# Optimization experiments

Measured on AMD Instinct MI355X. Metric: run time of the kernel, lower is better.

## Reference

```python
import jax, jax.numpy as jnp
import numpy as np

DIM, NH, NKV = 1024, 16, 4
HD = DIM // NH  # 64
B, T = 2, 2048


def _rotary_freqs(seq_len, dim):
    inv_freq = 1.0 / (10000.0 ** (jnp.arange(0, dim, 2, dtype=jnp.float32) / dim))
    pos = jnp.arange(seq_len, dtype=jnp.float32)
    return pos[:, None] * inv_freq[None, :]  # [T, dim/2]


def _apply_rotary(x, freqs):
    # x: [B, H, T, HD]; freqs: [T, HD/2]
    x1, x2 = x[..., ::2], x[..., 1::2]
    cos, sin = jnp.cos(freqs), jnp.sin(freqs)
    # NOTE: faithful to source, second half is x1*sin - x2*cos (not +)
    return jnp.concatenate([x1 * cos - x2 * sin, x1 * sin - x2 * cos], axis=-1)


def setup_inputs() -> dict:
    key = jax.random.key(0)
    ks = jax.random.split(key, 5)
    s = 0.02
    return {
        "x": jax.random.normal(ks[0], (B, T, DIM), dtype=jnp.float32),
        "Wq": jax.random.normal(ks[1], (DIM, DIM), dtype=jnp.float32) * s,
        "bq": jnp.zeros((DIM,), jnp.float32),
        "Wk": jax.random.normal(ks[2], (DIM, NKV * HD), dtype=jnp.float32) * s,
        "bk": jnp.zeros((NKV * HD,), jnp.float32),
        "Wv": jax.random.normal(ks[3], (DIM, NKV * HD), dtype=jnp.float32) * s,
        "bv": jnp.zeros((NKV * HD,), jnp.float32),
        "Wo": jax.random.normal(ks[4], (DIM, DIM), dtype=jnp.float32) * s,
        "bo": jnp.zeros((DIM,), jnp.float32),
    }


def reference(x, Wq, bq, Wk, bk, Wv, bv, Wo, bo):
    Bx, Tx, C = x.shape
    q = (x @ Wq + bq).reshape(Bx, Tx, NH, HD).transpose(0, 2, 1, 3)   # [B,NH,T,HD]
    k = (x @ Wk + bk).reshape(Bx, Tx, NKV, HD).transpose(0, 2, 1, 3)  # [B,NKV,T,HD]
    v = (x @ Wv + bv).reshape(Bx, Tx, NKV, HD).transpose(0, 2, 1, 3)

    freqs = _rotary_freqs(Tx, HD)
    q = _apply_rotary(q, freqs)
    k = _apply_rotary(k, freqs)

    rep = NH // NKV
    k = jnp.repeat(k, rep, axis=1)  # [B,NH,T,HD]
    v = jnpp = jnp.repeat(v, rep, axis=1)

    scores = jnp.einsum('bhqd,bhkd->bhqk', q, k) / jnp.sqrt(jnp.float32(HD))
    causal = jnp.tril(jnp.ones((Tx, Tx), dtype=bool))
    scores = jnp.where(causal[None, None], scores, -jnp.inf)
    attn = jax.nn.softmax(scores, axis=-1)
    ctx = jnp.einsum('bhqk,bhkd->bhqd', attn, v)
    out = ctx.transpose(0, 2, 1, 3).reshape(Bx, Tx, C)
    return out @ Wo + bo
```

## Files before the change

### kernel.cpp

```cpp
#include <hip/hip_runtime.h>
#include <math.h>

#define DIM 1024
#define NH 16
#define NKV 4
#define HD 64
#define HALF 32
#define NB 2
#define SEQ 2048
#define KVD 256
#define MTOT 4096
#define QSCALE 0.18033688f
#define MBIAS 8.0f

typedef __bf16 bf16x8 __attribute__((ext_vector_type(8)));
typedef float f32x4 __attribute__((ext_vector_type(4)));
typedef unsigned short u16x8 __attribute__((ext_vector_type(8)));

#define MFMA16(a, b, c) __builtin_amdgcn_mfma_f32_16x16x32_bf16(a, b, c, 0, 0, 0)

__device__ __forceinline__ unsigned short f2bf(float f) {
    unsigned int u = __float_as_uint(f);
    u = (u + 0x7fffu + ((u >> 16) & 1u)) >> 16;
    return (unsigned short)u;
}

__device__ __forceinline__ unsigned cvt_pk(float lo, float hi) {
    unsigned r;
    asm("v_cvt_pk_bf16_f32 %0, %1, %2" : "=v"(r) : "v"(lo), "v"(hi));
    return r;
}

__device__ __forceinline__ void gll16(const unsigned short* g, unsigned short* l) {
    __builtin_amdgcn_global_load_lds((const __attribute__((address_space(1))) void*)g,
                                     (__attribute__((address_space(3))) void*)l, 16, 0, 0);
}

__global__ __launch_bounds__(256) void prep_kernel(
    const float* __restrict__ x,
    const float* __restrict__ Wq, const float* __restrict__ Wk,
    const float* __restrict__ Wv, const float* __restrict__ Wo,
    unsigned short* __restrict__ xb,
    unsigned short* __restrict__ qt, unsigned short* __restrict__ kt,
    unsigned short* __restrict__ vt, unsigned short* __restrict__ ot,
    float* __restrict__ cosb, float* __restrict__ sinb)
{
    __shared__ float tile[64][65];
    const int bx = blockIdx.x;
    const int tid = threadIdx.x;
    if (bx < 256) {
        int idx = bx * 256 + tid;
        int t = idx >> 5, d = idx & 31;
        float e = (float)(2 * d) / (float)HD;
        float invf = 1.0f / powf(10000.0f, e);
        float f = (float)t * invf;
        cosb[idx] = cosf(f);
        sinb[idx] = sinf(f);
    } else if (bx < 2304) {
        int i = ((bx - 256) * 256 + tid) * 8;
        float4 v0 = *(const float4*)&x[i];
        float4 v1 = *(const float4*)&x[i + 4];
        u16x8 o;
        o[0] = f2bf(v0.x); o[1] = f2bf(v0.y); o[2] = f2bf(v0.z); o[3] = f2bf(v0.w);
        o[4] = f2bf(v1.x); o[5] = f2bf(v1.y); o[6] = f2bf(v1.z); o[7] = f2bf(v1.w);
        *(u16x8*)&xb[i] = o;
    } else {
        int idx2 = bx - 2304;
        int z = idx2 >> 8, rem = idx2 & 255, xx = rem & 15, yy = rem >> 4;
        const float* W; unsigned short* Wt; int N;
        switch (z) {
            case 0: W = Wq; Wt = qt; N = DIM; break;
            case 1: W = Wk; Wt = kt; N = KVD; break;
            case 2: W = Wv; Wt = vt; N = KVD; break;
            default: W = Wo; Wt = ot; N = DIM; break;
        }
        const int n0 = xx * 64;
        if (n0 >= N) return;
        const int k0 = yy * 64;
        const int row = tid >> 2, coff = (tid & 3) * 16;
#pragma unroll
        for (int i = 0; i < 4; i++) {
            float4 v = *(const float4*)&W[(size_t)(k0 + row) * N + n0 + coff + i * 4];
            tile[row][coff + i * 4 + 0] = v.x; tile[row][coff + i * 4 + 1] = v.y;
            tile[row][coff + i * 4 + 2] = v.z; tile[row][coff + i * 4 + 3] = v.w;
        }
        __syncthreads();
        u16x8 a, b;
#pragma unroll
        for (int i = 0; i < 8; i++) a[i] = f2bf(tile[coff + i][row]);
#pragma unroll
        for (int i = 0; i < 8; i++) b[i] = f2bf(tile[coff + 8 + i][row]);
        *(u16x8*)&Wt[(size_t)(n0 + row) * DIM + k0 + coff] = a;
        *(u16x8*)&Wt[(size_t)(n0 + row) * DIM + k0 + coff + 8] = b;
    }
}

__global__ __launch_bounds__(256) void qkv_gemm_kernel(
    const unsigned short* __restrict__ xb,
    const unsigned short* __restrict__ wqt, const unsigned short* __restrict__ wkt,
    const unsigned short* __restrict__ wvt,
    const float* __restrict__ bq, const float* __restrict__ bk, const float* __restrict__ bv,
    const float* __restrict__ cosb, const float* __restrict__ sinb,
    unsigned short* __restrict__ qbuf, unsigned short* __restrict__ kbuf,
    unsigned short* __restrict__ vT)
{
    __shared__ unsigned short As[64 * 64];
    __shared__ unsigned short Bs[128 * 64];
    const int tid = threadIdx.x;
    const int lane = tid & 63, w = tid >> 6;
    const int l15 = lane & 15, lg = lane >> 4;
    const int bid = blockIdx.x;
    const int lid = (bid & 7) * 96 + (bid >> 3);
    const int m0 = (lid / 12) * 64;
    const int n0g = (lid % 12) * 128;

    const unsigned short* Wt; const float* bias; int n0, mode;
    if (n0g < DIM)            { Wt = wqt; bias = bq; n0 = n0g; mode = 0; }
    else if (n0g < DIM + KVD) { Wt = wkt; bias = bk; n0 = n0g - DIM; mode = 1; }
    else                      { Wt = wvt; bias = bv; n0 = n0g - DIM - KVD; mode = 2; }

    const int wr = w >> 1, wc = w & 1;

    f32x4 acc[2][4];
#pragma unroll
    for (int i = 0; i < 2; i++)
#pragma unroll
        for (int j = 0; j < 4; j++) acc[i][j] = (f32x4){0.f, 0.f, 0.f, 0.f};

    for (int k0 = 0; k0 < DIM; k0 += 64) {
        __syncthreads();
#pragma unroll
        for (int i = 0; i < 2; i++) {
            int S = i * 256 + tid;
            int r = S >> 3, qd = S & 7;
            gll16(xb + (size_t)(m0 + r) * DIM + k0 + ((qd ^ (r & 7)) * 8),
                  &As[(i * 256 + (tid & ~63)) * 8]);
        }
#pragma unroll
        for (int i = 0; i < 4; i++) {
            int S = i * 256 + tid;
            int r = S >> 3, qd = S & 7;
            gll16(Wt + (size_t)(n0 + r) * DIM + k0 + ((qd ^ (r & 7)) * 8),
                  &Bs[(i * 256 + (tid & ~63)) * 8]);
        }
        __syncthreads();
        bf16x8 af[2][2], bfr[4][2];
#pragma unroll
        for (int r = 0; r < 2; r++) {
            const int row = wr * 32 + r * 16 + l15;
#pragma unroll
            for (int kk = 0; kk < 2; kk++)
                af[r][kk] = *(const bf16x8*)&As[row * 64 + (((kk * 4 + lg) ^ (row & 7)) << 3)];
        }
#pragma unroll
        for (int c = 0; c < 4; c++) {
            const int row = wc * 64 + c * 16 + l15;
#pragma unroll
            for (int kk = 0; kk < 2; kk++)
                bfr[c][kk] = *(const bf16x8*)&Bs[row * 64 + (((kk * 4 + lg) ^ (row & 7)) << 3)];
        }
#pragma unroll
        for (int kk = 0; kk < 2; kk++)
#pragma unroll
            for (int r = 0; r < 2; r++)
#pragma unroll
                for (int c = 0; c < 4; c++)
                    acc[r][c] = MFMA16(af[r][kk], bfr[c][kk], acc[r][c]);
    }

    const int nloc = n0 + wc * 64;
    const bool even = (l15 & 1) == 0;
#pragma unroll
    for (int rt = 0; rt < 2; rt++) {
#pragma unroll
        for (int ct = 0; ct < 4; ct++) {
            const int c = ct * 16 + l15;
            const float bsv = bias[nloc + c];
            if (mode == 2) {
                const int col = nloc + c;
                const int khh = col >> 6, d = col & 63;
                const int bb = m0 >> 11;
                const int t = (m0 & (SEQ - 1)) + wr * 32 + rt * 16 + lg * 4;
                float v0 = acc[rt][ct][0] + bsv;
                float v1 = acc[rt][ct][1] + bsv;
                float v2 = acc[rt][ct][2] + bsv;
                float v3 = acc[rt][ct][3] + bsv;
                unsigned short* dst = vT + ((size_t)(bb * NKV + khh) * 64 + d) * SEQ + t;
                *(uint2*)dst = make_uint2(cvt_pk(v0, v1), cvt_pk(v2, v3));
            } else {
                const int p = c >> 1;
#pragma unroll
                for (int q = 0; q < 4; q++) {
                    const int mrow = m0 + wr * 32 + rt * 16 + lg * 4 + q;
                    float val = acc[rt][ct][q] + bsv;
                    float prt = __shfl_xor(val, 1);
                    const int t = mrow & (SEQ - 1);
                    float cs = cosb[t * HALF + p];
                    float sn = sinb[t * HALF + p];
                    float outv = even ? (val * cs - prt * sn) : (prt * sn - val * cs);
                    int outc = even ? p : (p + 32);
                    if (mode == 0) qbuf[(size_t)mrow * DIM + nloc + outc] = f2bf(outv * QSCALE);
                    else           kbuf[(size_t)mrow * KVD + nloc + outc] = f2bf(outv);
                }
            }
        }
    }
}

__global__ __launch_bounds__(256, 4) void attn_mfma_kernel(
    const unsigned short* __restrict__ qb, const unsigned short* __restrict__ kb,
    const unsigned short* __restrict__ vT, unsigned short* __restrict__ ctx)
{
    __shared__ unsigned short Ks[2][64 * 64];
    __shared__ unsigned short Vt[2][64 * 64];
    __shared__ unsigned Pw[4][16 * 32];

    const int tid = threadIdx.x;
    const int lane = tid & 63, w = tid >> 6;
    const int l15 = lane & 15, lg = lane >> 4;
    const int h = blockIdx.y;
    const int b = blockIdx.z;
    const int kh = h >> 2;
    const int g = h + NH * b;
    const int v = (blockIdx.x + g) & 31;
    const int r_ = v & 7, k_ = v >> 3;
    const int tile = (k_ == 0) ? r_ : (k_ == 1) ? (r_ + 8) : (k_ == 2) ? (31 - r_) : (23 - r_);
    const int q0 = tile * 64;

    const unsigned short* kg = kb + (size_t)b * SEQ * KVD + (size_t)kh * HD;
    const unsigned short* vg = vT + ((size_t)(b * NKV + kh) * HD) * SEQ;

    const int qg_row = w * 16 + l15;
    const int swzd = (l15 & 7) << 3;
    unsigned* PW = &Pw[w][l15 * 32];
    const int pswz = (l15 & 7) << 2;

    const unsigned short* qptr = qb + ((size_t)(b * SEQ + q0 + qg_row) * DIM + h * HD + lg * 8);
    bf16x8 bq0 = *(const bf16x8*)qptr;
    bf16x8 bq1 = *(const bf16x8*)(qptr + 32);

    const int S1 = w * 64 + lane, r1 = S1 >> 3, d81 = ((S1 & 7) ^ (r1 & 7)) * 8;
    const int S2 = 256 + w * 64 + lane, r2 = S2 >> 3, d82 = ((S2 & 7) ^ (r2 & 7)) * 8;

    gll16(kg + (size_t)r1 * KVD + d81, &Ks[0][(w * 64) * 8]);
    gll16(vg + (size_t)r1 * SEQ + d81, &Vt[0][(w * 64) * 8]);
    gll16(kg + (size_t)r2 * KVD + d82, &Ks[0][(256 + w * 64) * 8]);
    gll16(vg + (size_t)r2 * SEQ + d82, &Vt[0][(256 + w * 64) * 8]);
    __syncthreads();

    f32x4 o[4];
#pragma unroll
    for (int i = 0; i < 4; i++) o[i] = (f32x4){0.f, 0.f, 0.f, 0.f};
    float lrun = 0.f;

    const int nch = tile + 1;
#pragma unroll 1
    for (int ch = 0; ch < nch; ch++) {
        const int cur = ch & 1;
        if (ch + 1 < nch) {
            const int kv1 = (ch + 1) * 64;
            gll16(kg + (size_t)(kv1 + r1) * KVD + d81, &Ks[cur ^ 1][(w * 64) * 8]);
            gll16(vg + (size_t)r1 * SEQ + kv1 + d81,   &Vt[cur ^ 1][(w * 64) * 8]);
            gll16(kg + (size_t)(kv1 + r2) * KVD + d82, &Ks[cur ^ 1][(256 + w * 64) * 8]);
            gll16(vg + (size_t)r2 * SEQ + kv1 + d82,   &Vt[cur ^ 1][(256 + w * 64) * 8]);
        }

        f32x4 sacc[4];
#pragma unroll
        for (int i = 0; i < 4; i++) sacc[i] = (f32x4){0.f, 0.f, 0.f, 0.f};
        __builtin_amdgcn_s_setprio(1);
#pragma unroll
        for (int ct = 0; ct < 4; ct++) {
            const int kr = ct * 16 + l15;
            bf16x8 ak = *(const bf16x8*)&Ks[cur][kr * 64 + ((lg * 8) ^ swzd)];
            sacc[ct] = MFMA16(ak, bq0, sacc[ct]);
        }
#pragma unroll
        for (int ct = 0; ct < 4; ct++) {
            const int kr = ct * 16 + l15;
            bf16x8 ak = *(const bf16x8*)&Ks[cur][kr * 64 + ((32 + lg * 8) ^ swzd)];
            sacc[ct] = MFMA16(ak, bq1, sacc[ct]);
        }
        __builtin_amdgcn_s_setprio(0);

        if (ch == nch - 1) {
#pragma unroll
            for (int ct = 0; ct < 4; ct++)
#pragma unroll
                for (int r = 0; r < 4; r++)
                    if (ct * 16 + lg * 4 + r > qg_row) sacc[ct][r] = -INFINITY;
        }

        float rs = 0.f;
        unsigned pk0[4], pk1[4];
#pragma unroll
        for (int ct = 0; ct < 4; ct++) {
            float p0 = exp2f(sacc[ct][0] - MBIAS);
            float p1 = exp2f(sacc[ct][1] - MBIAS);
            float p2 = exp2f(sacc[ct][2] - MBIAS);
            float p3 = exp2f(sacc[ct][3] - MBIAS);
            rs += (p0 + p1) + (p2 + p3);
            pk0[ct] = cvt_pk(p0, p1);
            pk1[ct] = cvt_pk(p2, p3);
        }
        lrun += rs;

#pragma unroll
        for (int ct = 0; ct < 4; ct++) {
            int wrd = (ct * 8 + lg * 2) ^ pswz;
            *(uint2*)&PW[wrd] = make_uint2(pk0[ct], pk1[ct]);
        }

        __builtin_amdgcn_s_setprio(1);
#pragma unroll
        for (int s = 0; s < 2; s++) {
            int wrd = (s * 16 + lg * 4) ^ pswz;
            bf16x8 ap = *(const bf16x8*)&PW[wrd];
#pragma unroll
            for (int dt = 0; dt < 4; dt++) {
                const int d = dt * 16 + l15;
                bf16x8 bv2 = *(const bf16x8*)&Vt[cur][d * 64 + ((s * 32 + lg * 8) ^ ((d & 7) << 3))];
                o[dt] = MFMA16(ap, bv2, o[dt]);
            }
        }
        __builtin_amdgcn_s_setprio(0);

        __syncthreads();
    }

    lrun += __shfl_xor(lrun, 16);
    lrun += __shfl_xor(lrun, 32);
    float linv = 1.0f / lrun;
    float lb0 = __shfl(linv, lg * 4 + 0);
    float lb1 = __shfl(linv, lg * 4 + 1);
    float lb2 = __shfl(linv, lg * 4 + 2);
    float lb3 = __shfl(linv, lg * 4 + 3);
#pragma unroll
    for (int dt = 0; dt < 4; dt++) {
        const size_t base = (size_t)(b * SEQ + q0 + w * 16 + lg * 4) * DIM + h * HD + dt * 16 + l15;
        ctx[base]           = f2bf(o[dt][0] * lb0);
        ctx[base + DIM]     = f2bf(o[dt][1] * lb1);
        ctx[base + 2 * DIM] = f2bf(o[dt][2] * lb2);
        ctx[base + 3 * DIM] = f2bf(o[dt][3] * lb3);
    }
}

__global__ __launch_bounds__(256) void outproj_kernel(
    const unsigned short* __restrict__ ctx, const unsigned short* __restrict__ wot,
    const float* __restrict__ bo, float* __restrict__ out)
{
    __shared__ unsigned short As[64 * 64];
    __shared__ unsigned short Bs[128 * 64];
    const int tid = threadIdx.x;
    const int lane = tid & 63, w = tid >> 6;
    const int l15 = lane & 15, lg = lane >> 4;
    const int bid = blockIdx.x;
    const int lid = (bid & 7) * 64 + (bid >> 3);
    const int m0 = (lid >> 3) * 64;
    const int n0 = (lid & 7) * 128;
    const int wr = w >> 1, wc = w & 1;

    f32x4 acc[2][4];
#pragma unroll
    for (int i = 0; i < 2; i++)
#pragma unroll
        for (int j = 0; j < 4; j++) acc[i][j] = (f32x4){0.f, 0.f, 0.f, 0.f};

    for (int k0 = 0; k0 < DIM; k0 += 64) {
        __syncthreads();
#pragma unroll
        for (int i = 0; i < 2; i++) {
            int S = i * 256 + tid;
            int r = S >> 3, qd = S & 7;
            gll16(ctx + (size_t)(m0 + r) * DIM + k0 + ((qd ^ (r & 7)) * 8),
                  &As[(i * 256 + (tid & ~63)) * 8]);
        }
#pragma unroll
        for (int i = 0; i < 4; i++) {
            int S = i * 256 + tid;
            int r = S >> 3, qd = S & 7;
            gll16(wot + (size_t)(n0 + r) * DIM + k0 + ((qd ^ (r & 7)) * 8),
                  &Bs[(i * 256 + (tid & ~63)) * 8]);
        }
        __syncthreads();
        bf16x8 af[2][2], bfr[4][2];
#pragma unroll
        for (int r = 0; r < 2; r++) {
            const int row = wr * 32 + r * 16 + l15;
#pragma unroll
            for (int kk = 0; kk < 2; kk++)
                af[r][kk] = *(const bf16x8*)&As[row * 64 + (((kk * 4 + lg) ^ (row & 7)) << 3)];
        }
#pragma unroll
        for (int c = 0; c < 4; c++) {
            const int row = wc * 64 + c * 16 + l15;
#pragma unroll
            for (int kk = 0; kk < 2; kk++)
                bfr[c][kk] = *(const bf16x8*)&Bs[row * 64 + (((kk * 4 + lg) ^ (row & 7)) << 3)];
        }
#pragma unroll
        for (int kk = 0; kk < 2; kk++)
#pragma unroll
            for (int r = 0; r < 2; r++)
#pragma unroll
                for (int c = 0; c < 4; c++)
                    acc[r][c] = MFMA16(af[r][kk], bfr[c][kk], acc[r][c]);
    }

#pragma unroll
    for (int rt = 0; rt < 2; rt++) {
#pragma unroll
        for (int ct = 0; ct < 4; ct++) {
            const int ncol = n0 + wc * 64 + ct * 16 + l15;
            const float bsv = bo[ncol];
#pragma unroll
            for (int q = 0; q < 4; q++) {
                const int mrow = m0 + wr * 32 + rt * 16 + lg * 4 + q;
                out[(size_t)mrow * DIM + ncol] = acc[rt][ct][q] + bsv;
            }
        }
    }
}

extern "C" void kernel_launch(void* const* d_in, const int* in_sizes, int n_in,
                              void* d_out, int out_size, void* d_ws, size_t ws_size,
                              hipStream_t stream) {
    (void)in_sizes; (void)n_in; (void)out_size; (void)ws_size;
    const float* x  = (const float*)d_in[0];
    const float* Wq = (const float*)d_in[1];
    const float* bq = (const float*)d_in[2];
    const float* Wk = (const float*)d_in[3];
    const float* bk = (const float*)d_in[4];
    const float* Wv = (const float*)d_in[5];
    const float* bv = (const float*)d_in[6];
    const float* Wo = (const float*)d_in[7];
    const float* bo = (const float*)d_in[8];
    float* out = (float*)d_out;
    char* ws = (char*)d_ws;

    unsigned short* xb  = (unsigned short*)(ws);
    unsigned short* qbf = (unsigned short*)(ws + 8388608);
    unsigned short* kbf = (unsigned short*)(ws + 16777216);
    unsigned short* ctx = (unsigned short*)(ws + 20971520);
    unsigned short* wqt = (unsigned short*)(ws + 29360128);
    unsigned short* wkt = (unsigned short*)(ws + 31457280);
    unsigned short* wvt = (unsigned short*)(ws + 31981568);
    unsigned short* wot = (unsigned short*)(ws + 32505856);
    float* cosb = (float*)(ws + 34603008);
    float* sinb = (float*)(ws + 34865152);
    unsigned short* vTb = (unsigned short*)(ws + 35127296);

    hipLaunchKernelGGL(prep_kernel, dim3(3328), dim3(256), 0, stream,
                       x, Wq, Wk, Wv, Wo, xb, wqt, wkt, wvt, wot, cosb, sinb);
    hipLaunchKernelGGL(qkv_gemm_kernel, dim3(768), dim3(256), 0, stream,
                       xb, wqt, wkt, wvt, bq, bk, bv, cosb, sinb, qbf, kbf, vTb);
    hipLaunchKernelGGL(attn_mfma_kernel, dim3(32, NH, NB), dim3(256), 0, stream,
                       qbf, kbf, vTb, ctx);
    hipLaunchKernelGGL(outproj_kernel, dim3(512), dim3(256), 0, stream,
                       ctx, wot, bo, out);
}
```

Measured before the change: 92.34 us.

## Use 128-row query tiles with 8 waves sharing each K/V chunk

The attention kernel now has each block cover 128 query rows with 512 threads (8 waves) instead of 64 rows with 4 waves, halving the grid. Each K/V chunk loaded into shared memory is reused by twice as many waves, which cuts global K/V traffic and load instructions per thread. Waves whose rows lie fully before a chunk skip its compute via a causal check, and the tile-order swizzle is redone for 16 tiles. The cost is more idle waves per block on the diagonal chunks and fewer blocks for load balancing.

```diff
diff --git a/kernel.cpp b/kernel.cpp
--- a/kernel.cpp
+++ b/kernel.cpp
@@ -207,13 +207,13 @@
     }
 }
 
-__global__ __launch_bounds__(256, 4) void attn_mfma_kernel(
+__global__ __launch_bounds__(512) void attn_mfma_kernel(
     const unsigned short* __restrict__ qb, const unsigned short* __restrict__ kb,
     const unsigned short* __restrict__ vT, unsigned short* __restrict__ ctx)
 {
     __shared__ unsigned short Ks[2][64 * 64];
     __shared__ unsigned short Vt[2][64 * 64];
-    __shared__ unsigned Pw[4][16 * 32];
+    __shared__ unsigned Pw[8][16 * 32];
 
     const int tid = threadIdx.x;
     const int lane = tid & 63, w = tid >> 6;
@@ -222,30 +222,26 @@
     const int b = blockIdx.z;
     const int kh = h >> 2;
     const int g = h + NH * b;
-    const int v = (blockIdx.x + g) & 31;
-    const int r_ = v & 7, k_ = v >> 3;
-    const int tile = (k_ == 0) ? r_ : (k_ == 1) ? (r_ + 8) : (k_ == 2) ? (31 - r_) : (23 - r_);
-    const int q0 = tile * 64;
+    const int v = (blockIdx.x + g + 8 * (g >> 4)) & 15;
+    const int T = (v >> 3) ? (15 - (v & 7)) : v;
+    const int q0 = T * 128;
 
     const unsigned short* kg = kb + (size_t)b * SEQ * KVD + (size_t)kh * HD;
     const unsigned short* vg = vT + ((size_t)(b * NKV + kh) * HD) * SEQ;
 
-    const int qg_row = w * 16 + l15;
+    const int qg_row = q0 + 16 * w + l15;
     const int swzd = (l15 & 7) << 3;
     unsigned* PW = &Pw[w][l15 * 32];
     const int pswz = (l15 & 7) << 2;
 
-    const unsigned short* qptr = qb + ((size_t)(b * SEQ + q0 + qg_row) * DIM + h * HD + lg * 8);
+    const unsigned short* qptr = qb + (size_t)(b * SEQ + qg_row) * DIM + h * HD + lg * 8;
     bf16x8 bq0 = *(const bf16x8*)qptr;
     bf16x8 bq1 = *(const bf16x8*)(qptr + 32);
 
-    const int S1 = w * 64 + lane, r1 = S1 >> 3, d81 = ((S1 & 7) ^ (r1 & 7)) * 8;
-    const int S2 = 256 + w * 64 + lane, r2 = S2 >> 3, d82 = ((S2 & 7) ^ (r2 & 7)) * 8;
+    const int r1 = tid >> 3, d81 = ((tid & 7) ^ (r1 & 7)) * 8;
 
     gll16(kg + (size_t)r1 * KVD + d81, &Ks[0][(w * 64) * 8]);
     gll16(vg + (size_t)r1 * SEQ + d81, &Vt[0][(w * 64) * 8]);
-    gll16(kg + (size_t)r2 * KVD + d82, &Ks[0][(256 + w * 64) * 8]);
-    gll16(vg + (size_t)r2 * SEQ + d82, &Vt[0][(256 + w * 64) * 8]);
     __syncthreads();
 
     f32x4 o[4];
@@ -253,7 +249,9 @@
     for (int i = 0; i < 4; i++) o[i] = (f32x4){0.f, 0.f, 0.f, 0.f};
     float lrun = 0.f;
 
-    const int nch = tile + 1;
+    const int nch = 2 * T + 2;
+    const int wmax = q0 + 16 * w + 15;
+    const int wmin = q0 + 16 * w;
 #pragma unroll 1
     for (int ch = 0; ch < nch; ch++) {
         const int cur = ch & 1;
@@ -261,69 +259,69 @@
             const int kv1 = (ch + 1) * 64;
             gll16(kg + (size_t)(kv1 + r1) * KVD + d81, &Ks[cur ^ 1][(w * 64) * 8]);
             gll16(vg + (size_t)r1 * SEQ + kv1 + d81,   &Vt[cur ^ 1][(w * 64) * 8]);
-            gll16(kg + (size_t)(kv1 + r2) * KVD + d82, &Ks[cur ^ 1][(256 + w * 64) * 8]);
-            gll16(vg + (size_t)r2 * SEQ + kv1 + d82,   &Vt[cur ^ 1][(256 + w * 64) * 8]);
-        }
-
-        f32x4 sacc[4];
-#pragma unroll
-        for (int i = 0; i < 4; i++) sacc[i] = (f32x4){0.f, 0.f, 0.f, 0.f};
-        __builtin_amdgcn_s_setprio(1);
-#pragma unroll
-        for (int ct = 0; ct < 4; ct++) {
-            const int kr = ct * 16 + l15;
-            bf16x8 ak = *(const bf16x8*)&Ks[cur][kr * 64 + ((lg * 8) ^ swzd)];
-            sacc[ct] = MFMA16(ak, bq0, sacc[ct]);
-        }
-#pragma unroll
-        for (int ct = 0; ct < 4; ct++) {
-            const int kr = ct * 16 + l15;
-            bf16x8 ak = *(const bf16x8*)&Ks[cur][kr * 64 + ((32 + lg * 8) ^ swzd)];
-            sacc[ct] = MFMA16(ak, bq1, sacc[ct]);
-        }
-        __builtin_amdgcn_s_setprio(0);
-
-        if (ch == nch - 1) {
-#pragma unroll
-            for (int ct = 0; ct < 4; ct++)
-#pragma unroll
-                for (int r = 0; r < 4; r++)
-                    if (ct * 16 + lg * 4 + r > qg_row) sacc[ct][r] = -INFINITY;
-        }
-
-        float rs = 0.f;
-        unsigned pk0[4], pk1[4];
-#pragma unroll
-        for (int ct = 0; ct < 4; ct++) {
-            float p0 = exp2f(sacc[ct][0] - MBIAS);
-            float p1 = exp2f(sacc[ct][1] - MBIAS);
-            float p2 = exp2f(sacc[ct][2] - MBIAS);
-            float p3 = exp2f(sacc[ct][3] - MBIAS);
-            rs += (p0 + p1) + (p2 + p3);
-            pk0[ct] = cvt_pk(p0, p1);
-            pk1[ct] = cvt_pk(p2, p3);
-        }
-        lrun += rs;
-
-#pragma unroll
-        for (int ct = 0; ct < 4; ct++) {
-            int wrd = (ct * 8 + lg * 2) ^ pswz;
-            *(uint2*)&PW[wrd] = make_uint2(pk0[ct], pk1[ct]);
-        }
-
-        __builtin_amdgcn_s_setprio(1);
-#pragma unroll
-        for (int s = 0; s < 2; s++) {
-            int wrd = (s * 16 + lg * 4) ^ pswz;
-            bf16x8 ap = *(const bf16x8*)&PW[wrd];
-#pragma unroll
-            for (int dt = 0; dt < 4; dt++) {
-                const int d = dt * 16 + l15;
-                bf16x8 bv2 = *(const bf16x8*)&Vt[cur][d * 64 + ((s * 32 + lg * 8) ^ ((d & 7) << 3))];
-                o[dt] = MFMA16(ap, bv2, o[dt]);
-            }
-        }
-        __builtin_amdgcn_s_setprio(0);
+        }
+
+        if (64 * ch <= wmax) {
+            f32x4 sacc[4];
+#pragma unroll
+            for (int i = 0; i < 4; i++) sacc[i] = (f32x4){0.f, 0.f, 0.f, 0.f};
+            __builtin_amdgcn_s_setprio(1);
+#pragma unroll
+            for (int ct = 0; ct < 4; ct++) {
+                const int kr = ct * 16 + l15;
+                bf16x8 ak = *(const bf16x8*)&Ks[cur][kr * 64 + ((lg * 8) ^ swzd)];
+                sacc[ct] = MFMA16(ak, bq0, sacc[ct]);
+            }
+#pragma unroll
+            for (int ct = 0; ct < 4; ct++) {
+                const int kr = ct * 16 + l15;
+                bf16x8 ak = *(const bf16x8*)&Ks[cur][kr * 64 + ((32 + lg * 8) ^ swzd)];
+                sacc[ct] = MFMA16(ak, bq1, sacc[ct]);
+            }
+            __builtin_amdgcn_s_setprio(0);
+
+            if (64 * ch + 63 > wmin) {
+#pragma unroll
+                for (int ct = 0; ct < 4; ct++)
+#pragma unroll
+                    for (int r = 0; r < 4; r++)
+                        if (64 * ch + ct * 16 + lg * 4 + r > qg_row) sacc[ct][r] = -INFINITY;
+            }
+
+            float rs = 0.f;
+            unsigned pk0[4], pk1[4];
+#pragma unroll
+            for (int ct = 0; ct < 4; ct++) {
+                float p0 = exp2f(sacc[ct][0] - MBIAS);
+                float p1 = exp2f(sacc[ct][1] - MBIAS);
+                float p2 = exp2f(sacc[ct][2] - MBIAS);
+                float p3 = exp2f(sacc[ct][3] - MBIAS);
+                rs += (p0 + p1) + (p2 + p3);
+                pk0[ct] = cvt_pk(p0, p1);
+                pk1[ct] = cvt_pk(p2, p3);
+            }
+            lrun += rs;
+
+#pragma unroll
+            for (int ct = 0; ct < 4; ct++) {
+                int wrd = (ct * 8 + lg * 2) ^ pswz;
+                *(uint2*)&PW[wrd] = make_uint2(pk0[ct], pk1[ct]);
+            }
+
+            __builtin_amdgcn_s_setprio(1);
+#pragma unroll
+            for (int s = 0; s < 2; s++) {
+                int wrd = (s * 16 + lg * 4) ^ pswz;
+                bf16x8 ap = *(const bf16x8*)&PW[wrd];
+#pragma unroll
+                for (int dt = 0; dt < 4; dt++) {
+                    const int d = dt * 16 + l15;
+                    bf16x8 bv2 = *(const bf16x8*)&Vt[cur][d * 64 + ((s * 32 + lg * 8) ^ ((d & 7) << 3))];
+                    o[dt] = MFMA16(ap, bv2, o[dt]);
+                }
+            }
+            __builtin_amdgcn_s_setprio(0);
+        }
 
         __syncthreads();
     }
@@ -337,7 +335,7 @@
     float lb3 = __shfl(linv, lg * 4 + 3);
 #pragma unroll
     for (int dt = 0; dt < 4; dt++) {
-        const size_t base = (size_t)(b * SEQ + q0 + w * 16 + lg * 4) * DIM + h * HD + dt * 16 + l15;
+        const size_t base = (size_t)(b * SEQ + q0 + 16 * w + lg * 4) * DIM + h * HD + dt * 16 + l15;
         ctx[base]           = f2bf(o[dt][0] * lb0);
         ctx[base + DIM]     = f2bf(o[dt][1] * lb1);
         ctx[base + 2 * DIM] = f2bf(o[dt][2] * lb2);
@@ -454,7 +452,7 @@
                        x, Wq, Wk, Wv, Wo, xb, wqt, wkt, wvt, wot, cosb, sinb);
     hipLaunchKernelGGL(qkv_gemm_kernel, dim3(768), dim3(256), 0, stream,
                        xb, wqt, wkt, wvt, bq, bk, bv, cosb, sinb, qbf, kbf, vTb);
-    hipLaunchKernelGGL(attn_mfma_kernel, dim3(32, NH, NB), dim3(256), 0, stream,
+    hipLaunchKernelGGL(attn_mfma_kernel, dim3(16, NH, NB), dim3(512), 0, stream,
                        qbf, kbf, vTb, ctx);
     hipLaunchKernelGGL(outproj_kernel, dim3(512), dim3(256), 0, stream,
                        ctx, wot, bo, out);
```

After: 95.49 us. 3.4% more time.

## Peel last causal chunk and use partial vmcnt waits for KV prefetch

Applied to the files above, without the earlier changes.

Restructures the attention KV loop so the final, masked chunk is peeled out of the main loop. The main loop runs without the mask branch. The loop now issues the next chunk's global-to-LDS loads and then waits only for the previous chunk's loads (vmcnt(4)) before an s_barrier, replacing the full __syncthreads that drained all outstanding memory ops. This is meant to overlap prefetch with compute. The risk is correctness if the vmcnt accounting does not match the number of outstanding loads, and extra code size from the duplicated tail.

```diff
diff --git a/kernel.cpp b/kernel.cpp
--- a/kernel.cpp
+++ b/kernel.cpp
@@ -246,7 +246,6 @@
     gll16(vg + (size_t)r1 * SEQ + d81, &Vt[0][(w * 64) * 8]);
     gll16(kg + (size_t)r2 * KVD + d82, &Ks[0][(256 + w * 64) * 8]);
     gll16(vg + (size_t)r2 * SEQ + d82, &Vt[0][(256 + w * 64) * 8]);
-    __syncthreads();
 
     f32x4 o[4];
 #pragma unroll
@@ -255,15 +254,17 @@
 
     const int nch = tile + 1;
 #pragma unroll 1
-    for (int ch = 0; ch < nch; ch++) {
+    for (int ch = 0; ch < nch - 1; ch++) {
         const int cur = ch & 1;
-        if (ch + 1 < nch) {
-            const int kv1 = (ch + 1) * 64;
-            gll16(kg + (size_t)(kv1 + r1) * KVD + d81, &Ks[cur ^ 1][(w * 64) * 8]);
-            gll16(vg + (size_t)r1 * SEQ + kv1 + d81,   &Vt[cur ^ 1][(w * 64) * 8]);
-            gll16(kg + (size_t)(kv1 + r2) * KVD + d82, &Ks[cur ^ 1][(256 + w * 64) * 8]);
-            gll16(vg + (size_t)r2 * SEQ + kv1 + d82,   &Vt[cur ^ 1][(256 + w * 64) * 8]);
-        }
+        const int kv1 = (ch + 1) * 64;
+        gll16(kg + (size_t)(kv1 + r1) * KVD + d81, &Ks[cur ^ 1][(w * 64) * 8]);
+        gll16(vg + (size_t)r1 * SEQ + kv1 + d81,   &Vt[cur ^ 1][(w * 64) * 8]);
+        gll16(kg + (size_t)(kv1 + r2) * KVD + d82, &Ks[cur ^ 1][(256 + w * 64) * 8]);
+        gll16(vg + (size_t)r2 * SEQ + kv1 + d82,   &Vt[cur ^ 1][(256 + w * 64) * 8]);
+
+        asm volatile("s_waitcnt vmcnt(4)" ::: "memory");
+        __builtin_amdgcn_s_barrier();
+        __builtin_amdgcn_sched_barrier(0);
 
         f32x4 sacc[4];
 #pragma unroll
@@ -282,14 +283,6 @@
             sacc[ct] = MFMA16(ak, bq1, sacc[ct]);
         }
         __builtin_amdgcn_s_setprio(0);
-
-        if (ch == nch - 1) {
-#pragma unroll
-            for (int ct = 0; ct < 4; ct++)
-#pragma unroll
-                for (int r = 0; r < 4; r++)
-                    if (ct * 16 + lg * 4 + r > qg_row) sacc[ct][r] = -INFINITY;
-        }
 
         float rs = 0.f;
         unsigned pk0[4], pk1[4];
@@ -325,7 +318,73 @@
         }
         __builtin_amdgcn_s_setprio(0);
 
-        __syncthreads();
+        asm volatile("" ::: "memory");
+        __builtin_amdgcn_s_barrier();
+        asm volatile("" ::: "memory");
+    }
+
+    {
+        const int cur = (nch - 1) & 1;
+        asm volatile("s_waitcnt vmcnt(0)" ::: "memory");
+        __builtin_amdgcn_s_barrier();
+        __builtin_amdgcn_sched_barrier(0);
+
+        f32x4 sacc[4];
+#pragma unroll
+        for (int i = 0; i < 4; i++) sacc[i] = (f32x4){0.f, 0.f, 0.f, 0.f};
+        __builtin_amdgcn_s_setprio(1);
+#pragma unroll
+        for (int ct = 0; ct < 4; ct++) {
+            const int kr = ct * 16 + l15;
+            bf16x8 ak = *(const bf16x8*)&Ks[cur][kr * 64 + ((lg * 8) ^ swzd)];
+            sacc[ct] = MFMA16(ak, bq0, sacc[ct]);
+        }
+#pragma unroll
+        for (int ct = 0; ct < 4; ct++) {
+            const int kr = ct * 16 + l15;
+            bf16x8 ak = *(const bf16x8*)&Ks[cur][kr * 64 + ((32 + lg * 8) ^ swzd)];
+            sacc[ct] = MFMA16(ak, bq1, sacc[ct]);
+        }
+        __builtin_amdgcn_s_setprio(0);
+
+#pragma unroll
+        for (int ct = 0; ct < 4; ct++)
+#pragma unroll
+            for (int r = 0; r < 4; r++)
+                if (ct * 16 + lg * 4 + r > qg_row) sacc[ct][r] = -INFINITY;
+
+        float rs = 0.f;
+        unsigned pk0[4], pk1[4];
+#pragma unroll
+        for (int ct = 0; ct < 4; ct++) {
+            float p0 = exp2f(sacc[ct][0] - MBIAS);
+            float p1 = exp2f(sacc[ct][1] - MBIAS);
+            float p2 = exp2f(sacc[ct][2] - MBIAS);
+            float p3 = exp2f(sacc[ct][3] - MBIAS);
+            rs += (p0 + p1) + (p2 + p3);
+            pk0[ct] = cvt_pk(p0, p1);
+            pk1[ct] = cvt_pk(p2, p3);
+        }
+        lrun += rs;
+#pragma unroll
+        for (int ct = 0; ct < 4; ct++) {
+            int wrd = (ct * 8 + lg * 2) ^ pswz;
+            *(uint2*)&PW[wrd] = make_uint2(pk0[ct], pk1[ct]);
+        }
+
+        __builtin_amdgcn_s_setprio(1);
+#pragma unroll
+        for (int s = 0; s < 2; s++) {
+            int wrd = (s * 16 + lg * 4) ^ pswz;
+            bf16x8 ap = *(const bf16x8*)&PW[wrd];
+#pragma unroll
+            for (int dt = 0; dt < 4; dt++) {
+                const int d = dt * 16 + l15;
+                bf16x8 bv2 = *(const bf16x8*)&Vt[cur][d * 64 + ((s * 32 + lg * 8) ^ ((d & 7) << 3))];
+                o[dt] = MFMA16(ap, bv2, o[dt]);
+            }
+        }
+        __builtin_amdgcn_s_setprio(0);
     }
 
     lrun += __shfl_xor(lrun, 16);
```

After: 93.35 us. Within noise of the previous version (+1.1%).
